# Performance work log

Measured on AMD Instinct MI355X. Metric: run time of the kernel, lower is better.

Reference implementation:

```python
import jax, jax.numpy as jnp
import numpy as np

N, D = 2048, 1024
H, KV, HD = 16, 4, 64
REPEATS = H // KV
SCALE = HD ** -0.5


def setup_inputs() -> dict:
    key = jax.random.key(0)
    ks = jax.random.split(key, 6)
    x = jax.random.normal(ks[0], (N, D), dtype=jnp.float32)
    # rotary tables: cos/sin of interleaved-pair angles (llama-style view_as_complex)
    pos = jnp.arange(N, dtype=jnp.float32)[:, None]
    inv_freq = 1.0 / (10000.0 ** (jnp.arange(0, HD, 2, dtype=jnp.float32) / HD))
    ang = pos * inv_freq[None, :]  # (N, HD//2)
    freqs_cos = jnp.cos(ang)
    freqs_sin = jnp.sin(ang)
    s = 0.02
    Wq = jax.random.normal(ks[1], (D, H * HD), dtype=jnp.float32) * s
    Wk = jax.random.normal(ks[2], (D, KV * HD), dtype=jnp.float32) * s
    Wv = jax.random.normal(ks[3], (D, KV * HD), dtype=jnp.float32) * s
    Wo = jax.random.normal(ks[4], (H * HD, D), dtype=jnp.float32) * s
    return {"x": x, "freqs_cos": freqs_cos, "freqs_sin": freqs_sin,
            "Wq": Wq, "Wk": Wk, "Wv": Wv, "Wo": Wo}


def _rope(t, cos, sin):
    # t: (N, heads, HD); interleaved complex pairs (even=real, odd=imag)
    tr = t[..., 0::2]
    ti = t[..., 1::2]
    c = cos[:, None, :]
    s = sin[:, None, :]
    out_r = tr * c - ti * s
    out_i = tr * s + ti * c
    return jnp.stack([out_r, out_i], axis=-1).reshape(t.shape)


def reference(x, freqs_cos, freqs_sin, Wq, Wk, Wv, Wo):
    n = x.shape[0]
    xq = (x @ Wq).reshape(n, H, HD)
    xk = (x @ Wk).reshape(n, KV, HD)
    xv = (x @ Wv).reshape(n, KV, HD)
    xq = _rope(xq, freqs_cos, freqs_sin)
    xk = _rope(xk, freqs_cos, freqs_sin)
    # repeat_kv along head dim (GQA)
    k = jnp.repeat(xk, REPEATS, axis=1)  # (n, H, HD)
    v = jnp.repeat(xv, REPEATS, axis=1)
    # memory_efficient_attention with mask=None: full attention over token axis
    scores = jnp.einsum('nhd,mhd->hnm', xq, k) * SCALE
    attn = jax.nn.softmax(scores, axis=-1)
    out = jnp.einsum('hnm,mhd->nhd', attn, v)
    return out.reshape(n, H * HD) @ Wo
```

## Files before the change

### kernel.cpp

```cpp
#include <hip/hip_runtime.h>

#define N_TOK 2048
#define DMODEL 1024
#define NH 16
#define NKV 4
#define HDIM 64
#define SCALE_LOG2E 0.1803368801111204f

typedef __attribute__((ext_vector_type(8))) short short8;
typedef __attribute__((ext_vector_type(4))) float f32x4;
typedef __attribute__((ext_vector_type(16))) float f32x16;
typedef unsigned short u16;
typedef unsigned int u32;

__device__ __forceinline__ u16 f2bf(float x) {
    u32 u = __float_as_uint(x);
    u += 0x7FFF + ((u >> 16) & 1);
    return (u16)(u >> 16);
}
__device__ __forceinline__ u32 pack2(float a, float b) {
    return (u32)f2bf(a) | ((u32)f2bf(b) << 16);
}
__device__ __forceinline__ u32 pack2t(float a, float b) {
    return __builtin_amdgcn_perm(__float_as_uint(b), __float_as_uint(a), 0x07060302u);
}

__global__ __launch_bounds__(256) void prep(
    const float* __restrict__ Wq, const float* __restrict__ Wk,
    const float* __restrict__ Wv, const float* __restrict__ Wo,
    const float* __restrict__ x,
    u16* __restrict__ Wqt, u16* __restrict__ Wkt, u16* __restrict__ Wvt,
    u16* __restrict__ Wot, u16* __restrict__ xb)
{
    const int z = blockIdx.z;
    const int t = threadIdx.x;
    if (z == 4) {
        size_t base = ((size_t)(blockIdx.y * 16 + blockIdx.x)) * 8192;
#pragma unroll
        for (int i = 0; i < 8; ++i) {
            float4 v = *(const float4*)(x + base + i * 1024 + t * 4);
            uint2 p; p.x = pack2(v.x, v.y); p.y = pack2(v.z, v.w);
            *(uint2*)(xb + base + i * 1024 + t * 4) = p;
        }
        return;
    }
    const float* W; u16* Wt; int NC;
    if      (z == 0) { W = Wq; Wt = Wqt; NC = 1024; }
    else if (z == 1) { W = Wk; Wt = Wkt; NC = 256; }
    else if (z == 2) { W = Wv; Wt = Wvt; NC = 256; }
    else             { W = Wo; Wt = Wot; NC = 1024; }
    const int n0 = blockIdx.x * 64;
    if (n0 >= NC) return;
    const int k0 = blockIdx.y * 64;
    __shared__ float T[64][68];
    const int row = t >> 2, cs = (t & 3) * 16;
#pragma unroll
    for (int i = 0; i < 4; ++i)
        *(float4*)&T[row][cs + i * 4] =
            *(const float4*)(W + (size_t)(k0 + row) * NC + n0 + cs + i * 4);
    __syncthreads();
    const int nl = t >> 2, ks = (t & 3) * 16;
    u32 pk[8];
#pragma unroll
    for (int i = 0; i < 8; ++i)
        pk[i] = pack2(T[ks + 2 * i][nl], T[ks + 2 * i + 1][nl]);
    u16* dst = Wt + (size_t)(n0 + nl) * DMODEL + k0 + ks;
    uint4 w0; w0.x = pk[0]; w0.y = pk[1]; w0.z = pk[2]; w0.w = pk[3];
    uint4 w1; w1.x = pk[4]; w1.y = pk[5]; w1.z = pk[6]; w1.w = pk[7];
    *(uint4*)(dst) = w0;
    *(uint4*)(dst + 8) = w1;
}

__global__ __launch_bounds__(256, 3) void gemm_qkv(
    const u16* __restrict__ A,
    const u16* __restrict__ B0, const u16* __restrict__ B1, const u16* __restrict__ B2,
    u16* __restrict__ D0, u16* __restrict__ D1, u16* __restrict__ FVout,
    const float* __restrict__ fc, const float* __restrict__ fs)
{
    __shared__ u16 As[64][40];
    __shared__ u16 Bs[64][40];
    const int t = threadIdx.x;
    const int m0 = blockIdx.x * 64;
    const int by = blockIdx.y;

    const u16* Bt; int nl0, ep;
    u16* dbf = nullptr; int dstride = 0; float epsc = 1.f;
    if (by < 16)      { Bt = B0; nl0 = by * 64;        dbf = D0; ep = 1; dstride = 1024;
                        epsc = SCALE_LOG2E; }
    else if (by < 20) { Bt = B1; nl0 = (by - 16) * 64; dbf = D1; ep = 1; dstride = 256; }
    else              { Bt = B2; nl0 = (by - 20) * 64; ep = 2; }

    const int w = t >> 6, lane = t & 63;
    const int quad = lane >> 4, l15 = lane & 15;
    const int wm = (w >> 1) * 32, wn = (w & 1) * 32;
    const int srow = t >> 2, sk = (t & 3) * 8;

    const u16* Ap = A + (size_t)(m0 + srow) * DMODEL + sk;
    const u16* Bp = Bt + (size_t)(nl0 + srow) * DMODEL + sk;

    f32x4 acc[2][2];
#pragma unroll
    for (int i = 0; i < 2; ++i)
#pragma unroll
        for (int j = 0; j < 2; ++j) acc[i][j] = {0.f, 0.f, 0.f, 0.f};

    uint4 ar = *(const uint4*)(Ap);
    uint4 br = *(const uint4*)(Bp);

    for (int k0 = 0; k0 < DMODEL; k0 += 32) {
        __syncthreads();
        *(uint4*)&As[srow][sk] = ar;
        *(uint4*)&Bs[srow][sk] = br;
        __syncthreads();
        if (k0 + 32 < DMODEL) {
            ar = *(const uint4*)(Ap + k0 + 32);
            br = *(const uint4*)(Bp + k0 + 32);
        }
        short8 af[2], bf[2];
#pragma unroll
        for (int i = 0; i < 2; ++i)
            af[i] = *(const short8*)&As[wm + i * 16 + l15][quad * 8];
#pragma unroll
        for (int j = 0; j < 2; ++j)
            bf[j] = *(const short8*)&Bs[wn + j * 16 + l15][quad * 8];
#pragma unroll
        for (int i = 0; i < 2; ++i)
#pragma unroll
            for (int j = 0; j < 2; ++j)
                acc[i][j] = __builtin_amdgcn_mfma_f32_16x16x32_bf16(af[i], bf[j], acc[i][j], 0, 0, 0);
    }

#pragma unroll
    for (int i = 0; i < 2; ++i)
#pragma unroll
        for (int j = 0; j < 2; ++j) {
            const int cl = nl0 + wn + j * 16 + l15;
#pragma unroll
            for (int r4 = 0; r4 < 4; ++r4) {
                const int r = m0 + wm + i * 16 + quad * 4 + r4;
                float own = acc[i][j][r4];
                if (ep == 1) {
                    float other = __shfl_xor(own, 1, 64);
                    const int p = (cl & 63) >> 1;
                    const float c = fc[r * 32 + p] * epsc, s = fs[r * 32 + p] * epsc;
                    float outv = ((cl & 1) == 0) ? (own * c - other * s)
                                                 : (other * s + own * c);
                    dbf[(size_t)r * dstride + cl] = f2bf(outv);
                } else {
                    const int g = cl >> 6, d = cl & 63;
                    const int d2 = d >> 5, dl = d & 31;
                    const int keyblk = r >> 7, kg = (r >> 5) & 3;
                    const int kst = (r >> 4) & 1, hb = (r >> 3) & 1, jv = r & 7;
                    size_t idx = ((((((size_t)(g * 16 + keyblk) * 4 + kg) * 2 + kst) * 2 + d2)
                                   * 2 + hb) * 32 + dl) * 8 + jv;
                    FVout[idx] = f2bf(own);
                }
            }
        }
}

__global__ __launch_bounds__(256, 2) void gemm_out(
    const u16* __restrict__ A, const u16* __restrict__ Bt, float* __restrict__ Dout)
{
    __shared__ u16 As[64][40];
    __shared__ u16 Bs[64][40];
    const int t = threadIdx.x;
    const int m0 = blockIdx.x * 64;
    const int nl0 = blockIdx.y * 64;

    const int w = t >> 6, lane = t & 63;
    const int quad = lane >> 4, l15 = lane & 15;
    const int wm = (w >> 1) * 32, wn = (w & 1) * 32;
    const int srow = t >> 2, sk = (t & 3) * 8;

    const u16* Ap = A + (size_t)(m0 + srow) * DMODEL + sk;
    const u16* Bp = Bt + (size_t)(nl0 + srow) * DMODEL + sk;

    f32x4 acc[2][2];
#pragma unroll
    for (int i = 0; i < 2; ++i)
#pragma unroll
        for (int j = 0; j < 2; ++j) acc[i][j] = {0.f, 0.f, 0.f, 0.f};

    uint4 ar = *(const uint4*)(Ap);
    uint4 br = *(const uint4*)(Bp);

    for (int k0 = 0; k0 < DMODEL; k0 += 32) {
        __syncthreads();
        *(uint4*)&As[srow][sk] = ar;
        *(uint4*)&Bs[srow][sk] = br;
        __syncthreads();
        if (k0 + 32 < DMODEL) {
            ar = *(const uint4*)(Ap + k0 + 32);
            br = *(const uint4*)(Bp + k0 + 32);
        }
        short8 af[2], bf[2];
#pragma unroll
        for (int i = 0; i < 2; ++i)
            af[i] = *(const short8*)&As[wm + i * 16 + l15][quad * 8];
#pragma unroll
        for (int j = 0; j < 2; ++j)
            bf[j] = *(const short8*)&Bs[wn + j * 16 + l15][quad * 8];
#pragma unroll
        for (int i = 0; i < 2; ++i)
#pragma unroll
            for (int j = 0; j < 2; ++j)
                acc[i][j] = __builtin_amdgcn_mfma_f32_16x16x32_bf16(af[i], bf[j], acc[i][j], 0, 0, 0);
    }

#pragma unroll
    for (int i = 0; i < 2; ++i)
#pragma unroll
        for (int j = 0; j < 2; ++j) {
            const int cl = nl0 + wn + j * 16 + l15;
#pragma unroll
            for (int r4 = 0; r4 < 4; ++r4) {
                const int r = m0 + wm + i * 16 + quad * 4 + r4;
                Dout[(size_t)r * 1024 + cl] = acc[i][j][r4];
            }
        }
}

__global__ __launch_bounds__(256, 2) void attn_part(
    const u16* __restrict__ Qb, const u16* __restrict__ Kb,
    const u16* __restrict__ FV, float* __restrict__ Opart, float* __restrict__ Lpart)
{
    __shared__ u16 Ks[2][128][72];
    __shared__ u16 Ps[4][32][40];

    const int t = threadIdx.x;
    const int n0 = blockIdx.x * 128;
    const int h = blockIdx.y, kvh = h >> 2;
    const int ksp = blockIdx.z;
    const int w = t >> 6, lane = t & 63;
    const int hi = lane >> 5, l31 = lane & 31;
    const int srow = t >> 1, ssel = (t & 1) * 32;

    const u16* qp = Qb + (size_t)(n0 + w * 32 + l31) * (NH * HDIM) + h * HDIM + hi * 8;
    short8 qf[4];
#pragma unroll
    for (int s = 0; s < 4; ++s) qf[s] = *(const short8*)(qp + s * 16);

    const u16* kbase = Kb + (size_t)(ksp * 1024 + srow) * (NKV * HDIM) + kvh * HDIM + ssel;
    const u16* fvb = FV + ((size_t)kvh * 16 * 8192) + (size_t)lane * 8;

    f32x16 o[2];
#pragma unroll
    for (int d2 = 0; d2 < 2; ++d2)
#pragma unroll
        for (int r = 0; r < 16; ++r) o[d2][r] = 0.f;
    float l_acc = 0.f;

#pragma unroll
    for (int c = 0; c < 4; ++c)
        *(uint4*)&Ks[0][srow][ssel + c * 8] = *(const uint4*)(kbase + c * 8);
    __syncthreads();

    for (int rd = 0; rd < 8; ++rd) {
        const int cur = rd & 1, nxt = cur ^ 1;
        const int rdn = (rd + 1) & 7;
        uint4 kr[4];
#pragma unroll
        for (int c = 0; c < 4; ++c)
            kr[c] = *(const uint4*)(kbase + (size_t)(rdn * 128) * (NKV * HDIM) + c * 8);
        const int keyblk = ksp * 8 + rd;

#pragma unroll
        for (int kg = 0; kg < 4; ++kg) {
            short8 vf[2][2];
#pragma unroll
            for (int s = 0; s < 2; ++s)
#pragma unroll
                for (int d2 = 0; d2 < 2; ++d2)
                    vf[s][d2] = *(const short8*)(fvb +
                        ((((size_t)keyblk * 4 + kg) * 2 + s) * 2 + d2) * 512);
            f32x16 sa;
#pragma unroll
            for (int r = 0; r < 16; ++r) sa[r] = 0.f;
#pragma unroll
            for (int s = 0; s < 4; ++s) {
                short8 kf = *(const short8*)&Ks[cur][kg * 32 + l31][s * 16 + hi * 8];
                sa = __builtin_amdgcn_mfma_f32_32x32x16_bf16(kf, qf[s], sa, 0, 0, 0);
            }
            float p[16];
#pragma unroll
            for (int r = 0; r < 16; ++r) p[r] = __builtin_amdgcn_exp2f(sa[r]);
            l_acc += ((p[0] + p[1]) + (p[2] + p[3])) + ((p[4] + p[5]) + (p[6] + p[7]))
                   + ((p[8] + p[9]) + (p[10] + p[11])) + ((p[12] + p[13]) + (p[14] + p[15]));
#pragma unroll
            for (int blk = 0; blk < 4; ++blk) {
                uint2 pk;
                pk.x = pack2t(p[blk * 4 + 0], p[blk * 4 + 1]);
                pk.y = pack2t(p[blk * 4 + 2], p[blk * 4 + 3]);
                *(uint2*)&Ps[w][l31][blk * 8 + 4 * hi] = pk;
            }
            const short8 ap0 = *(const short8*)&Ps[w][l31][hi * 8];
            const short8 ap1 = *(const short8*)&Ps[w][l31][16 + hi * 8];
#pragma unroll
            for (int d2 = 0; d2 < 2; ++d2) {
                o[d2] = __builtin_amdgcn_mfma_f32_32x32x16_bf16(ap0, vf[0][d2], o[d2], 0, 0, 0);
                o[d2] = __builtin_amdgcn_mfma_f32_32x32x16_bf16(ap1, vf[1][d2], o[d2], 0, 0, 0);
            }
        }
#pragma unroll
        for (int c = 0; c < 4; ++c)
            *(uint4*)&Ks[nxt][srow][ssel + c * 8] = kr[c];
        __syncthreads();
    }

    l_acc += __shfl_xor(l_acc, 32, 64);
    if (lane < 32)
        Lpart[(size_t)ksp * (NH * N_TOK) + h * N_TOK + n0 + w * 32 + lane] = l_acc;
    float* op = Opart + (size_t)ksp * N_TOK * 1024;
#pragma unroll
    for (int d2 = 0; d2 < 2; ++d2)
#pragma unroll
        for (int r = 0; r < 16; ++r) {
            const int q = n0 + w * 32 + (r & 3) + 8 * (r >> 2) + 4 * hi;
            op[(size_t)q * 1024 + h * HDIM + d2 * 32 + l31] = o[d2][r];
        }
}

__global__ __launch_bounds__(256) void combine(
    const float* __restrict__ Opart, const float* __restrict__ Lpart,
    u16* __restrict__ aob)
{
    const int row = blockIdx.x, t = threadIdx.x;
    const int h = t >> 4;
    const float4 a = *(const float4*)(Opart + (size_t)row * 1024 + t * 4);
    const float4 b = *(const float4*)(Opart + (size_t)N_TOK * 1024 + (size_t)row * 1024 + t * 4);
    const float li = 1.f / (Lpart[h * N_TOK + row] + Lpart[NH * N_TOK + h * N_TOK + row]);
    uint2 ov;
    ov.x = pack2((a.x + b.x) * li, (a.y + b.y) * li);
    ov.y = pack2((a.z + b.z) * li, (a.w + b.w) * li);
    *(uint2*)(aob + (size_t)row * 1024 + t * 4) = ov;
}

extern "C" void kernel_launch(void* const* d_in, const int* in_sizes, int n_in,
                              void* d_out, int out_size, void* d_ws, size_t ws_size,
                              hipStream_t stream) {
    const float* x  = (const float*)d_in[0];
    const float* fc = (const float*)d_in[1];
    const float* fs = (const float*)d_in[2];
    const float* Wq = (const float*)d_in[3];
    const float* Wk = (const float*)d_in[4];
    const float* Wv = (const float*)d_in[5];
    const float* Wo = (const float*)d_in[6];
    float* out = (float*)d_out;

    u16* ws  = (u16*)d_ws;
    u16* xb  = ws;
    u16* Wqt = xb  + (size_t)2048 * 1024;
    u16* Wkt = Wqt + (size_t)1024 * 1024;
    u16* Wvt = Wkt + (size_t)256 * 1024;
    u16* Wot = Wvt + (size_t)256 * 1024;
    u16* qb  = Wot + (size_t)1024 * 1024;
    u16* kb  = qb  + (size_t)2048 * 1024;
    u16* fv  = kb  + (size_t)2048 * 256;
    u16* aob = fv  + (size_t)256 * 2048;
    float* opart = (float*)(aob + (size_t)2048 * 1024);
    float* lpart = opart + (size_t)2 * 2048 * 1024;

    prep<<<dim3(16, 16, 5), dim3(256), 0, stream>>>(Wq, Wk, Wv, Wo, x,
                                                    Wqt, Wkt, Wvt, Wot, xb);
    gemm_qkv<<<dim3(32, 24), dim3(256), 0, stream>>>(xb, Wqt, Wkt, Wvt,
                                                     qb, kb, fv, fc, fs);
    attn_part<<<dim3(16, 16, 2), dim3(256), 0, stream>>>(qb, kb, fv, opart, lpart);
    combine<<<dim3(2048), dim3(256), 0, stream>>>(opart, lpart, aob);
    gemm_out<<<dim3(32, 16), dim3(256), 0, stream>>>(aob, Wot, out);
}
```

Measured before the change: 138.1 us.

## Double-buffer LDS in QKV and output GEMMs with larger K and M tiles

Both projection GEMMs now use double-buffered shared memory with a 64-wide K step, so there is one barrier per iteration instead of two and the next tile's global loads overlap the current MFMAs. The QKV GEMM also doubles its M tile to 128 rows per block, giving each wave 4x2 MFMA tiles for more B reuse. Its V-layout epilogue now packs four bf16 values into a single 8-byte store. In exchange the QKV grid halves to 384 blocks, and the larger LDS and register footprint lowers occupancy (launch bounds go from 3 to 2).

Result: no change. 136.8 us (-0.9%).

```diff
diff --git a/kernel.cpp b/kernel.cpp
--- a/kernel.cpp
+++ b/kernel.cpp
@@ -71,16 +71,16 @@
     *(uint4*)(dst + 8) = w1;
 }
 
-__global__ __launch_bounds__(256, 3) void gemm_qkv(
+__global__ __launch_bounds__(256, 2) void gemm_qkv(
     const u16* __restrict__ A,
     const u16* __restrict__ B0, const u16* __restrict__ B1, const u16* __restrict__ B2,
     u16* __restrict__ D0, u16* __restrict__ D1, u16* __restrict__ FVout,
     const float* __restrict__ fc, const float* __restrict__ fs)
 {
-    __shared__ u16 As[64][40];
-    __shared__ u16 Bs[64][40];
+    __shared__ u16 As[2][128][72];
+    __shared__ u16 Bs[2][64][72];
     const int t = threadIdx.x;
-    const int m0 = blockIdx.x * 64;
+    const int m0 = blockIdx.x * 128;
     const int by = blockIdx.y;
 
     const u16* Bt; int nl0, ep;
@@ -92,69 +92,94 @@
 
     const int w = t >> 6, lane = t & 63;
     const int quad = lane >> 4, l15 = lane & 15;
-    const int wm = (w >> 1) * 32, wn = (w & 1) * 32;
-    const int srow = t >> 2, sk = (t & 3) * 8;
-
-    const u16* Ap = A + (size_t)(m0 + srow) * DMODEL + sk;
-    const u16* Bp = Bt + (size_t)(nl0 + srow) * DMODEL + sk;
-
-    f32x4 acc[2][2];
-#pragma unroll
-    for (int i = 0; i < 2; ++i)
+    const int wm = (w >> 1) * 64, wn = (w & 1) * 32;
+    const int arow = t >> 1, ac = (t & 1) * 32;
+    const int brow = t >> 2, bc = (t & 3) * 16;
+
+    const u16* Ap = A + (size_t)(m0 + arow) * DMODEL + ac;
+    const u16* Bp = Bt + (size_t)(nl0 + brow) * DMODEL + bc;
+
+    f32x4 acc[4][2];
+#pragma unroll
+    for (int i = 0; i < 4; ++i)
 #pragma unroll
         for (int j = 0; j < 2; ++j) acc[i][j] = {0.f, 0.f, 0.f, 0.f};
 
-    uint4 ar = *(const uint4*)(Ap);
-    uint4 br = *(const uint4*)(Bp);
-
-    for (int k0 = 0; k0 < DMODEL; k0 += 32) {
-        __syncthreads();
-        *(uint4*)&As[srow][sk] = ar;
-        *(uint4*)&Bs[srow][sk] = br;
-        __syncthreads();
-        if (k0 + 32 < DMODEL) {
-            ar = *(const uint4*)(Ap + k0 + 32);
-            br = *(const uint4*)(Bp + k0 + 32);
-        }
-        short8 af[2], bf[2];
-#pragma unroll
-        for (int i = 0; i < 2; ++i)
-            af[i] = *(const short8*)&As[wm + i * 16 + l15][quad * 8];
-#pragma unroll
-        for (int j = 0; j < 2; ++j)
-            bf[j] = *(const short8*)&Bs[wn + j * 16 + l15][quad * 8];
-#pragma unroll
-        for (int i = 0; i < 2; ++i)
+    uint4 a_r[4], b_r[2];
+#pragma unroll
+    for (int ci = 0; ci < 4; ++ci) a_r[ci] = *(const uint4*)(Ap + ci * 8);
+    b_r[0] = *(const uint4*)(Bp);
+    b_r[1] = *(const uint4*)(Bp + 8);
+#pragma unroll
+    for (int ci = 0; ci < 4; ++ci) *(uint4*)&As[0][arow][ac + ci * 8] = a_r[ci];
+    *(uint4*)&Bs[0][brow][bc]     = b_r[0];
+    *(uint4*)&Bs[0][brow][bc + 8] = b_r[1];
+    __syncthreads();
+
+    for (int it = 0; it < 16; ++it) {
+        const int cur = it & 1;
+        const bool more = (it + 1) < 16;
+        if (more) {
+            const int k1 = (it + 1) * 64;
+#pragma unroll
+            for (int ci = 0; ci < 4; ++ci) a_r[ci] = *(const uint4*)(Ap + k1 + ci * 8);
+            b_r[0] = *(const uint4*)(Bp + k1);
+            b_r[1] = *(const uint4*)(Bp + k1 + 8);
+        }
+#pragma unroll
+        for (int c = 0; c < 2; ++c) {
+            short8 af[4], bf[2];
+#pragma unroll
+            for (int i = 0; i < 4; ++i)
+                af[i] = *(const short8*)&As[cur][wm + i * 16 + l15][c * 32 + quad * 8];
 #pragma unroll
             for (int j = 0; j < 2; ++j)
-                acc[i][j] = __builtin_amdgcn_mfma_f32_16x16x32_bf16(af[i], bf[j], acc[i][j], 0, 0, 0);
+                bf[j] = *(const short8*)&Bs[cur][wn + j * 16 + l15][c * 32 + quad * 8];
+#pragma unroll
+            for (int i = 0; i < 4; ++i)
+#pragma unroll
+                for (int j = 0; j < 2; ++j)
+                    acc[i][j] = __builtin_amdgcn_mfma_f32_16x16x32_bf16(af[i], bf[j], acc[i][j], 0, 0, 0);
+        }
+        if (more) {
+            const int nx = cur ^ 1;
+#pragma unroll
+            for (int ci = 0; ci < 4; ++ci) *(uint4*)&As[nx][arow][ac + ci * 8] = a_r[ci];
+            *(uint4*)&Bs[nx][brow][bc]     = b_r[0];
+            *(uint4*)&Bs[nx][brow][bc + 8] = b_r[1];
+            __syncthreads();
+        }
     }
 
 #pragma unroll
-    for (int i = 0; i < 2; ++i)
+    for (int i = 0; i < 4; ++i)
 #pragma unroll
         for (int j = 0; j < 2; ++j) {
             const int cl = nl0 + wn + j * 16 + l15;
-#pragma unroll
-            for (int r4 = 0; r4 < 4; ++r4) {
-                const int r = m0 + wm + i * 16 + quad * 4 + r4;
-                float own = acc[i][j][r4];
-                if (ep == 1) {
+            if (ep == 1) {
+#pragma unroll
+                for (int r4 = 0; r4 < 4; ++r4) {
+                    const int r = m0 + wm + i * 16 + quad * 4 + r4;
+                    float own = acc[i][j][r4];
                     float other = __shfl_xor(own, 1, 64);
                     const int p = (cl & 63) >> 1;
                     const float c = fc[r * 32 + p] * epsc, s = fs[r * 32 + p] * epsc;
                     float outv = ((cl & 1) == 0) ? (own * c - other * s)
                                                  : (other * s + own * c);
                     dbf[(size_t)r * dstride + cl] = f2bf(outv);
-                } else {
-                    const int g = cl >> 6, d = cl & 63;
-                    const int d2 = d >> 5, dl = d & 31;
-                    const int keyblk = r >> 7, kg = (r >> 5) & 3;
-                    const int kst = (r >> 4) & 1, hb = (r >> 3) & 1, jv = r & 7;
-                    size_t idx = ((((((size_t)(g * 16 + keyblk) * 4 + kg) * 2 + kst) * 2 + d2)
-                                   * 2 + hb) * 32 + dl) * 8 + jv;
-                    FVout[idx] = f2bf(own);
                 }
+            } else {
+                const int rb = m0 + wm + i * 16 + quad * 4;
+                const int g = cl >> 6, d = cl & 63;
+                const int d2 = d >> 5, dl = d & 31;
+                const int keyblk = rb >> 7, kg = (rb >> 5) & 3;
+                const int kst = (rb >> 4) & 1, hb = (rb >> 3) & 1, jv = rb & 7;
+                size_t idx = ((((((size_t)(g * 16 + keyblk) * 4 + kg) * 2 + kst) * 2 + d2)
+                               * 2 + hb) * 32 + dl) * 8 + jv;
+                uint2 pk;
+                pk.x = pack2(acc[i][j][0], acc[i][j][1]);
+                pk.y = pack2(acc[i][j][2], acc[i][j][3]);
+                *(uint2*)(FVout + idx) = pk;
             }
         }
 }
@@ -162,8 +187,8 @@
 __global__ __launch_bounds__(256, 2) void gemm_out(
     const u16* __restrict__ A, const u16* __restrict__ Bt, float* __restrict__ Dout)
 {
-    __shared__ u16 As[64][40];
-    __shared__ u16 Bs[64][40];
+    __shared__ u16 As[2][64][72];
+    __shared__ u16 Bs[2][64][72];
     const int t = threadIdx.x;
     const int m0 = blockIdx.x * 64;
     const int nl0 = blockIdx.y * 64;
@@ -171,7 +196,7 @@
     const int w = t >> 6, lane = t & 63;
     const int quad = lane >> 4, l15 = lane & 15;
     const int wm = (w >> 1) * 32, wn = (w & 1) * 32;
-    const int srow = t >> 2, sk = (t & 3) * 8;
+    const int srow = t >> 2, sk = (t & 3) * 16;
 
     const u16* Ap = A + (size_t)(m0 + srow) * DMODEL + sk;
     const u16* Bp = Bt + (size_t)(nl0 + srow) * DMODEL + sk;
@@ -182,30 +207,46 @@
 #pragma unroll
         for (int j = 0; j < 2; ++j) acc[i][j] = {0.f, 0.f, 0.f, 0.f};
 
-    uint4 ar = *(const uint4*)(Ap);
-    uint4 br = *(const uint4*)(Bp);
-
-    for (int k0 = 0; k0 < DMODEL; k0 += 32) {
-        __syncthreads();
-        *(uint4*)&As[srow][sk] = ar;
-        *(uint4*)&Bs[srow][sk] = br;
-        __syncthreads();
-        if (k0 + 32 < DMODEL) {
-            ar = *(const uint4*)(Ap + k0 + 32);
-            br = *(const uint4*)(Bp + k0 + 32);
-        }
-        short8 af[2], bf[2];
-#pragma unroll
-        for (int i = 0; i < 2; ++i)
-            af[i] = *(const short8*)&As[wm + i * 16 + l15][quad * 8];
-#pragma unroll
-        for (int j = 0; j < 2; ++j)
-            bf[j] = *(const short8*)&Bs[wn + j * 16 + l15][quad * 8];
-#pragma unroll
-        for (int i = 0; i < 2; ++i)
+    uint4 a_r[2], b_r[2];
+    a_r[0] = *(const uint4*)(Ap);     a_r[1] = *(const uint4*)(Ap + 8);
+    b_r[0] = *(const uint4*)(Bp);     b_r[1] = *(const uint4*)(Bp + 8);
+    *(uint4*)&As[0][srow][sk]     = a_r[0];
+    *(uint4*)&As[0][srow][sk + 8] = a_r[1];
+    *(uint4*)&Bs[0][srow][sk]     = b_r[0];
+    *(uint4*)&Bs[0][srow][sk + 8] = b_r[1];
+    __syncthreads();
+
+    for (int it = 0; it < 16; ++it) {
+        const int cur = it & 1;
+        const bool more = (it + 1) < 16;
+        if (more) {
+            const int k1 = (it + 1) * 64;
+            a_r[0] = *(const uint4*)(Ap + k1);     a_r[1] = *(const uint4*)(Ap + k1 + 8);
+            b_r[0] = *(const uint4*)(Bp + k1);     b_r[1] = *(const uint4*)(Bp + k1 + 8);
+        }
+#pragma unroll
+        for (int c = 0; c < 2; ++c) {
+            short8 af[2], bf[2];
+#pragma unroll
+            for (int i = 0; i < 2; ++i)
+                af[i] = *(const short8*)&As[cur][wm + i * 16 + l15][c * 32 + quad * 8];
 #pragma unroll
             for (int j = 0; j < 2; ++j)
-                acc[i][j] = __builtin_amdgcn_mfma_f32_16x16x32_bf16(af[i], bf[j], acc[i][j], 0, 0, 0);
+                bf[j] = *(const short8*)&Bs[cur][wn + j * 16 + l15][c * 32 + quad * 8];
+#pragma unroll
+            for (int i = 0; i < 2; ++i)
+#pragma unroll
+                for (int j = 0; j < 2; ++j)
+                    acc[i][j] = __builtin_amdgcn_mfma_f32_16x16x32_bf16(af[i], bf[j], acc[i][j], 0, 0, 0);
+        }
+        if (more) {
+            const int nx = cur ^ 1;
+            *(uint4*)&As[nx][srow][sk]     = a_r[0];
+            *(uint4*)&As[nx][srow][sk + 8] = a_r[1];
+            *(uint4*)&Bs[nx][srow][sk]     = b_r[0];
+            *(uint4*)&Bs[nx][srow][sk + 8] = b_r[1];
+            __syncthreads();
+        }
     }
 
 #pragma unroll
@@ -363,7 +404,7 @@
 
     prep<<<dim3(16, 16, 5), dim3(256), 0, stream>>>(Wq, Wk, Wv, Wo, x,
                                                     Wqt, Wkt, Wvt, Wot, xb);
-    gemm_qkv<<<dim3(32, 24), dim3(256), 0, stream>>>(xb, Wqt, Wkt, Wvt,
+    gemm_qkv<<<dim3(16, 24), dim3(256), 0, stream>>>(xb, Wqt, Wkt, Wvt,
                                                      qb, kb, fv, fc, fs);
     attn_part<<<dim3(16, 16, 2), dim3(256), 0, stream>>>(qb, kb, fv, opart, lpart);
     combine<<<dim3(2048), dim3(256), 0, stream>>>(opart, lpart, aob);
```
